# Kernel optimization log

Measured on AMD Instinct MI355X. Metric: run time of the kernel, lower is better.

The kernel has to match this reference:

```python
import math
import jax, jax.numpy as jnp
import numpy as np

D_MODEL = 1024
N_HEAD = 16
HEAD_DIM = D_MODEL // N_HEAD


def _alibi_slopes(n_heads: int) -> np.ndarray:
    def pow2_slopes(n):
        start = 2.0 ** (-(2.0 ** (-(math.log2(n) - 3))))
        return [start * (start ** i) for i in range(n)]
    if math.log2(n_heads).is_integer():
        slopes = pow2_slopes(n_heads)
    else:
        cp2 = 2 ** math.floor(math.log2(n_heads))
        slopes = pow2_slopes(cp2)
        slopes += pow2_slopes(2 * cp2)[0::2][: n_heads - cp2]
    return np.asarray(slopes, dtype=np.float32)


def setup_inputs() -> dict:
    key = jax.random.key(0)
    ks = jax.random.split(key, 12)
    B, N, D = 2, 2048, D_MODEL
    s = 1.0 / math.sqrt(D)
    inp = {
        "x_q": jax.random.normal(ks[0], (B, N, D), dtype=jnp.float32),
        "x_kv": jax.random.normal(ks[1], (B, N, D), dtype=jnp.float32),
        "attn_bias": jax.random.normal(ks[2], (N, N), dtype=jnp.float32) * 0.1,
        "Wq": jax.random.normal(ks[3], (D, D), dtype=jnp.float32) * s,
        "bq": jnp.zeros((D,), dtype=jnp.float32),
        "Wk": jax.random.normal(ks[4], (D, D), dtype=jnp.float32) * s,
        "bk": jnp.zeros((D,), dtype=jnp.float32),
        "Wv": jax.random.normal(ks[5], (D, D), dtype=jnp.float32) * s,
        "bv": jnp.zeros((D,), dtype=jnp.float32),
        "Wo": jax.random.normal(ks[6], (D, D), dtype=jnp.float32) * s,
        "bo": jnp.zeros((D,), dtype=jnp.float32),
        "is_self_attn": 1,
        "causal": 1,
    }
    return inp


def reference(x_q, x_kv, attn_bias, Wq, bq, Wk, bk, Wv, bv, Wo, bo, is_self_attn, causal):
    B, Nq, D = x_q.shape
    Nk = x_kv.shape[1]
    H, hd = N_HEAD, HEAD_DIM

    # torch Linear: y = x @ W.T + b
    q = (jnp.einsum("bqd,ed->bqe", x_q, Wq) + bq).reshape(B, Nq, H, hd)
    k = (jnp.einsum("bkd,ed->bke", x_kv, Wk) + bk).reshape(B, Nk, H, hd)
    v = (jnp.einsum("bkd,ed->bke", x_kv, Wv) + bv).reshape(B, Nk, H, hd)

    logits = jnp.einsum("bqhd,bkhd->bhqk", q, k) / math.sqrt(hd)  # [B,H,Nq,Nk]

    if is_self_attn and Nq == Nk:
        i = jnp.arange(Nq)[:, None]
        j = jnp.arange(Nk)[None, :]
        dist = jnp.maximum(j - i, 0).astype(jnp.float32)  # [Nq,Nk]
        slopes = jnp.asarray(_alibi_slopes(H))  # [H]
        logits = logits - slopes[None, :, None, None] * dist[None, None]

    if attn_bias is not None:
        logits = logits + attn_bias[None, None]

    if causal and is_self_attn and Nq == Nk:
        mask = jnp.triu(jnp.ones((Nq, Nk), dtype=bool), k=1)
        logits = jnp.where(mask[None, None], -jnp.inf, logits)

    attn = jax.nn.softmax(logits, axis=-1)
    out = jnp.einsum("bhqk,bkhd->bqhd", attn, v).reshape(B, Nq, D)
    return jnp.einsum("bqd,ed->bqe", out, Wo) + bo
```

## Files before the change

### kernel.cpp

```cpp
#include <hip/hip_runtime.h>
#include <hip/hip_bf16.h>

typedef __attribute__((ext_vector_type(8))) short short8;
typedef __attribute__((ext_vector_type(4))) float floatx4;

#define NSEQ   2048
#define DMODEL 1024
#define NHEAD  16
#define HDIM   64
#define BATCH  2
#define LOG2E 1.44269504088896340736f

#define XF4   1048576u
#define WF4   262144u

__device__ __forceinline__ void gload16(const void* g, void* l) {
    __builtin_amdgcn_global_load_lds(
        (const __attribute__((address_space(1))) void*)g,
        (__attribute__((address_space(3))) void*)l, 16, 0, 0);
}

#define BARRIER() asm volatile("s_barrier" ::: "memory")

__global__ __launch_bounds__(256)
void cvt_all(const float* __restrict__ xq, const float* __restrict__ xkv,
             const float* __restrict__ wq, const float* __restrict__ wk,
             const float* __restrict__ wv, const float* __restrict__ wo,
             __hip_bfloat16* __restrict__ dxq, __hip_bfloat16* __restrict__ dxkv,
             __hip_bfloat16* __restrict__ dwq, __hip_bfloat16* __restrict__ dwk,
             __hip_bfloat16* __restrict__ dwv, __hip_bfloat16* __restrict__ dwo)
{
    const unsigned total = 2*XF4 + 4*WF4;
    const unsigned stride = gridDim.x * blockDim.x;
    for (unsigned i = blockIdx.x*blockDim.x + threadIdx.x; i < total; i += stride) {
        const float4* src; __hip_bfloat16* dst; unsigned off;
        if (i < XF4)        { src = (const float4*)xq;  dst = dxq;  off = i; }
        else if (i < 2*XF4) { src = (const float4*)xkv; dst = dxkv; off = i - XF4; }
        else {
            unsigned j = i - 2*XF4; unsigned ws = j >> 18; off = j & (WF4 - 1);
            src = (const float4*)(ws==0 ? wq : ws==1 ? wk : ws==2 ? wv : wo);
            dst = (ws==0 ? dwq : ws==1 ? dwk : ws==2 ? dwv : dwo);
        }
        float4 v = src[off];
        __hip_bfloat16 h[4] = {__float2bfloat16(v.x), __float2bfloat16(v.y),
                               __float2bfloat16(v.z), __float2bfloat16(v.w)};
        *reinterpret_cast<uint2*>(dst + (size_t)off*4) = *reinterpret_cast<uint2*>(h);
    }
}

__global__ __launch_bounds__(256)
void cvt_bias(const float* __restrict__ src, __hip_bfloat16* __restrict__ dst)
{
    const unsigned total = (unsigned)(NSEQ*(size_t)NSEQ/4);
    const unsigned stride = gridDim.x * blockDim.x;
    for (unsigned i = blockIdx.x*blockDim.x + threadIdx.x; i < total; i += stride) {
        float4 v = ((const float4*)src)[i];
        __hip_bfloat16 h[4] = {__float2bfloat16(v.x), __float2bfloat16(v.y),
                               __float2bfloat16(v.z), __float2bfloat16(v.w)};
        *reinterpret_cast<uint2*>(dst + (size_t)i*4) = *reinterpret_cast<uint2*>(h);
    }
}

struct QkvArgs {
    const __hip_bfloat16* A[3];
    const __hip_bfloat16* W[3];
    const float*          bias[3];
    __hip_bfloat16*       out[3];
};

__global__ __launch_bounds__(256)
void qkv_gemm(QkvArgs args)
{
    __shared__ __hip_bfloat16 S[256][72];

    const int tid  = threadIdx.x;
    const int lane = tid & 63;
    const int wv   = tid >> 6;
    const int wm   = wv >> 1, wn = wv & 1;
    const int l15  = lane & 15, l4 = lane >> 4;
    const int m0   = blockIdx.x * 128;
    const int n0   = blockIdx.y * 128;
    const int z    = blockIdx.z;

    const __hip_bfloat16* __restrict__ A = args.A[z];
    const __hip_bfloat16* __restrict__ W = args.W[z];

    floatx4 acc[4][4] = {};

    for (int k0 = 0; k0 < DMODEL; k0 += 64) {
        #pragma unroll
        for (int it = 0; it < 4; ++it) {
            const int sI   = tid + 256 * it;
            const int row  = sI >> 2;
            const int colq = (sI & 3) * 16;
            const __hip_bfloat16* src = (it < 2)
                ? A + (size_t)(m0 + row) * DMODEL + k0 + colq
                : W + (size_t)(n0 + row - 128) * DMODEL + k0 + colq;
            const uint4* s4 = reinterpret_cast<const uint4*>(src);
            *reinterpret_cast<uint4*>(&S[row][colq])     = s4[0];
            *reinterpret_cast<uint4*>(&S[row][colq + 8]) = s4[1];
        }
        __syncthreads();

        #pragma unroll
        for (int kk = 0; kk < 64; kk += 32) {
            short8 af[4], bf[4];
            #pragma unroll
            for (int mi = 0; mi < 4; ++mi)
                af[mi] = *reinterpret_cast<const short8*>(&S[wm*64 + mi*16 + l15][kk + l4*8]);
            #pragma unroll
            for (int nj = 0; nj < 4; ++nj)
                bf[nj] = *reinterpret_cast<const short8*>(&S[128 + wn*64 + nj*16 + l15][kk + l4*8]);
            #pragma unroll
            for (int mi = 0; mi < 4; ++mi)
                #pragma unroll
                for (int nj = 0; nj < 4; ++nj)
                    acc[mi][nj] = __builtin_amdgcn_mfma_f32_16x16x32_bf16(
                        af[mi], bf[nj], acc[mi][nj], 0, 0, 0);
        }
        __syncthreads();
    }

    const float* bias = args.bias[z];
    __hip_bfloat16* C = args.out[z];
    const bool vt = (z == 2);
    #pragma unroll
    for (int mi = 0; mi < 4; ++mi) {
        const int mbase = m0 + wm*64 + mi*16 + l4*4;
        #pragma unroll
        for (int nj = 0; nj < 4; ++nj) {
            const int nn = n0 + wn*64 + nj*16 + l15;
            const float bb = bias[nn];
            const int h = nn >> 6, d = nn & (HDIM - 1);
            #pragma unroll
            for (int r = 0; r < 4; ++r) {
                const int m = mbase + r;
                const int b = m >> 11, n = m & (NSEQ - 1);
                const float val = acc[mi][nj][r] + bb;
                if (!vt)
                    C[((size_t)(b*NHEAD + h) * NSEQ + n) * HDIM + d] = __float2bfloat16(val);
                else
                    C[((size_t)(b*NHEAD + h) * HDIM + d) * NSEQ + n] = __float2bfloat16(val);
            }
        }
    }
}

__global__ __launch_bounds__(256)
void oproj_gemm(const __hip_bfloat16* __restrict__ A, const __hip_bfloat16* __restrict__ W,
                const float* __restrict__ bias, float* __restrict__ C)
{
    __shared__ __hip_bfloat16 S[192][72];

    const int tid  = threadIdx.x;
    const int lane = tid & 63;
    const int wv   = tid >> 6;
    const int l15  = lane & 15, l4 = lane >> 4;
    const int m0   = blockIdx.x * 64;
    const int n0   = blockIdx.y * 128;

    floatx4 acc[4][2] = {};

    for (int k0 = 0; k0 < DMODEL; k0 += 64) {
        #pragma unroll
        for (int it = 0; it < 3; ++it) {
            const int sI   = tid + 256 * it;
            const int row  = sI >> 2;
            const int colq = (sI & 3) * 16;
            const __hip_bfloat16* src = (it < 1)
                ? A + (size_t)(m0 + row) * DMODEL + k0 + colq
                : W + (size_t)(n0 + row - 64) * DMODEL + k0 + colq;
            const uint4* s4 = reinterpret_cast<const uint4*>(src);
            *reinterpret_cast<uint4*>(&S[row][colq])     = s4[0];
            *reinterpret_cast<uint4*>(&S[row][colq + 8]) = s4[1];
        }
        __syncthreads();

        #pragma unroll
        for (int kk = 0; kk < 64; kk += 32) {
            short8 af[4], bf[2];
            #pragma unroll
            for (int mi = 0; mi < 4; ++mi)
                af[mi] = *reinterpret_cast<const short8*>(&S[mi*16 + l15][kk + l4*8]);
            #pragma unroll
            for (int nj = 0; nj < 2; ++nj)
                bf[nj] = *reinterpret_cast<const short8*>(&S[64 + wv*32 + nj*16 + l15][kk + l4*8]);
            #pragma unroll
            for (int mi = 0; mi < 4; ++mi)
                #pragma unroll
                for (int nj = 0; nj < 2; ++nj)
                    acc[mi][nj] = __builtin_amdgcn_mfma_f32_16x16x32_bf16(
                        af[mi], bf[nj], acc[mi][nj], 0, 0, 0);
        }
        __syncthreads();
    }

    #pragma unroll
    for (int mi = 0; mi < 4; ++mi) {
        const int mbase = m0 + mi*16 + l4*4;
        #pragma unroll
        for (int nj = 0; nj < 2; ++nj) {
            const int nn = n0 + wv*32 + nj*16 + l15;
            const float bb = bias[nn];
            #pragma unroll
            for (int r = 0; r < 4; ++r)
                C[(size_t)(mbase + r) * DMODEL + nn] = acc[mi][nj][r] + bb;
        }
    }
}

__global__ __launch_bounds__(256)
void flash_attn(const __hip_bfloat16* __restrict__ Q,
                const __hip_bfloat16* __restrict__ K,
                const __hip_bfloat16* __restrict__ VT,
                const __hip_bfloat16* __restrict__ Bb,
                const int* __restrict__ selfp,
                const int* __restrict__ causalp,
                __hip_bfloat16* __restrict__ Oout)
{
    __shared__ __align__(16) char KB[2][8192];
    __shared__ __align__(16) char VB[2][8192];
    __shared__ __align__(16) char BBUF[2][8192];
    __shared__ __hip_bfloat16 pl[4][16][72];

    const int tid  = threadIdx.x;
    const int lane = tid & 63;
    const int wv   = tid >> 6;
    const int l15  = lane & 15, l4 = lane >> 4;

    const int g   = blockIdx.x;
    const int bh  = ((g >> 3) & 3) * 8 + (g & 7);
    const int m   = g >> 5;
    const int u   = m & 7, k2 = m >> 3;
    const int qb  = (k2==0) ? u : (k2==1) ? 31-u : (k2==2) ? 8+u : 23-u;
    const int h   = bh & (NHEAD - 1);
    const int b   = bh >> 4;

    const int selfF   = selfp[0];
    const int causalF = causalp[0];
    const bool cz      = (selfF != 0) && (causalF != 0);
    const bool alibiOn = (selfF != 0) && (causalF == 0);
    const float slopeL2 = exp2f(-(8.0f / NHEAD) * (float)(h + 1)) * LOG2E;

    const char* Kh = (const char*)(K  + (size_t)bh * NSEQ * HDIM);
    const char* Vh = (const char*)(VT + (size_t)bh * HDIM * NSEQ);
    const char* Bh = (const char*)(Bb + (size_t)qb * 64 * NSEQ);
    const __hip_bfloat16* Qh = Q + (size_t)bh * NSEQ * HDIM;

    const int q0 = qb*64 + wv*16;
    const short8 qf0 = *(const short8*)&Qh[(q0 + l15)*HDIM + l4*8];
    const short8 qf1 = *(const short8*)&Qh[(q0 + l15)*HDIM + 32 + l4*8];

    const int nt = cz ? (qb + 1) : (NSEQ/64);

    const int srow = lane >> 3;
    const int co   = (((lane & 7) ^ srow) << 4);

    auto stage = [&](int t, int bi) {
        const int j0 = t << 6;
        #pragma unroll
        for (int i2 = 0; i2 < 2; ++i2) {
            const int rl = wv*16 + i2*8 + srow;
            const int db = (wv*16 + i2*8) * 128;
            gload16(Kh + (size_t)(j0 + rl)*128 + co,          &KB[bi][db]);
            gload16(Vh + (size_t)rl*4096 + (size_t)j0*2 + co, &VB[bi][db]);
            gload16(Bh + (size_t)rl*4096 + (size_t)j0*2 + co, &BBUF[bi][db]);
        }
    };

    floatx4 o[4] = {};
    float lr[4] = {0.f, 0.f, 0.f, 0.f};

    stage(0, 0);
    int cur = 0;
    for (int t = 0; t < nt; ++t) {
        if (t + 1 < nt) {
            stage(t + 1, cur ^ 1);
            asm volatile("s_waitcnt vmcnt(6)" ::: "memory");
        } else {
            asm volatile("s_waitcnt vmcnt(0)" ::: "memory");
        }
        BARRIER();

        const char* kb = KB[cur];
        const char* vb = VB[cur];
        const char* bb = BBUF[cur];

        floatx4 s4[4];
        #pragma unroll
        for (int tt = 0; tt < 4; ++tt) {
            const int row = tt*16 + l15;
            const int sw  = (row & 7) << 4;
            const short8 kf0 = *(const short8*)(kb + ((row*128 + l4*16)      ^ sw));
            const short8 kf1 = *(const short8*)(kb + ((row*128 + 64 + l4*16) ^ sw));
            floatx4 z = {};
            z      = __builtin_amdgcn_mfma_f32_16x16x32_bf16(qf0, kf0, z, 0, 0, 0);
            s4[tt] = __builtin_amdgcn_mfma_f32_16x16x32_bf16(qf1, kf1, z, 0, 0, 0);
        }

        const bool domask = cz && (t == nt - 1);
        #pragma unroll
        for (int tt = 0; tt < 4; ++tt) {
            #pragma unroll
            for (int r = 0; r < 4; ++r) {
                const int qloc = wv*16 + l4*4 + r;
                const int jloc = tt*16 + l15;
                const int bbyte = (qloc*128 + jloc*2) ^ ((qloc & 7) << 4);
                const unsigned short ub = *(const unsigned short*)(bb + bbyte);
                union { unsigned int i; float f; } cvu; cvu.i = ((unsigned)ub) << 16;
                float v2 = fmaf(s4[tt][r], 0.125f * LOG2E, cvu.f * LOG2E);
                if (alibiOn) {
                    const int dd = (t*64 + jloc) - (qb*64 + qloc);
                    if (dd > 0) v2 = fmaf((float)dd, -slopeL2, v2);
                }
                float e = __builtin_amdgcn_exp2f(v2);
                if (domask && jloc > qloc) e = 0.0f;
                lr[r] += e;
                pl[wv][l4*4 + r][tt*16 + l15] = __float2bfloat16(e);
            }
        }

        const short8 pf0 = *(const short8*)&pl[wv][l15][l4*8];
        const short8 pf1 = *(const short8*)&pl[wv][l15][32 + l4*8];

        #pragma unroll
        for (int dt = 0; dt < 4; ++dt) {
            const int row = dt*16 + l15;
            const int sw  = (row & 7) << 4;
            const short8 vf0 = *(const short8*)(vb + ((row*128 + l4*16)      ^ sw));
            const short8 vf1 = *(const short8*)(vb + ((row*128 + 64 + l4*16) ^ sw));
            o[dt] = __builtin_amdgcn_mfma_f32_16x16x32_bf16(pf0, vf0, o[dt], 0, 0, 0);
            o[dt] = __builtin_amdgcn_mfma_f32_16x16x32_bf16(pf1, vf1, o[dt], 0, 0, 0);
        }

        BARRIER();
        cur ^= 1;
    }

    #pragma unroll
    for (int msk = 1; msk < 16; msk <<= 1)
        #pragma unroll
        for (int r = 0; r < 4; ++r)
            lr[r] += __shfl_xor(lr[r], msk);

    #pragma unroll
    for (int r = 0; r < 4; ++r) {
        const float inv = 1.0f / lr[r];
        const int n = qb*64 + wv*16 + l4*4 + r;
        #pragma unroll
        for (int dt = 0; dt < 4; ++dt)
            Oout[((size_t)(b*NSEQ + n)) * DMODEL + h*HDIM + dt*16 + l15] =
                __float2bfloat16(o[dt][r] * inv);
    }
}

extern "C" void kernel_launch(void* const* d_in, const int* in_sizes, int n_in,
                              void* d_out, int out_size, void* d_ws, size_t ws_size,
                              hipStream_t stream)
{
    (void)in_sizes; (void)n_in; (void)out_size; (void)ws_size;
    const float* x_q  = (const float*)d_in[0];
    const float* x_kv = (const float*)d_in[1];
    const float* ab   = (const float*)d_in[2];
    const float* Wq   = (const float*)d_in[3];
    const float* bq   = (const float*)d_in[4];
    const float* Wk   = (const float*)d_in[5];
    const float* bk   = (const float*)d_in[6];
    const float* Wv   = (const float*)d_in[7];
    const float* bv   = (const float*)d_in[8];
    const float* Wo   = (const float*)d_in[9];
    const float* bo   = (const float*)d_in[10];
    const int* selfp   = (const int*)d_in[11];
    const int* causalp = (const int*)d_in[12];

    const size_t XB = (size_t)BATCH * NSEQ * DMODEL * sizeof(__hip_bfloat16);
    const size_t WB = (size_t)DMODEL * DMODEL * sizeof(__hip_bfloat16);
    char* ws = (char*)d_ws;
    __hip_bfloat16* xq_b  = (__hip_bfloat16*)(ws);
    __hip_bfloat16* AO    = (__hip_bfloat16*)(ws);
    __hip_bfloat16* xkv_b = (__hip_bfloat16*)(ws + XB);
    __hip_bfloat16* ab_b  = (__hip_bfloat16*)(ws + XB);
    __hip_bfloat16* Wq_b  = (__hip_bfloat16*)(ws + 2*XB);
    __hip_bfloat16* Wk_b  = (__hip_bfloat16*)(ws + 2*XB + WB);
    __hip_bfloat16* Wv_b  = (__hip_bfloat16*)(ws + 2*XB + 2*WB);
    __hip_bfloat16* Wo_b  = (__hip_bfloat16*)(ws + 2*XB + 3*WB);
    __hip_bfloat16* Qb    = (__hip_bfloat16*)(ws + 2*XB + 4*WB);
    __hip_bfloat16* Kb    = (__hip_bfloat16*)(ws + 2*XB + 4*WB + XB);
    __hip_bfloat16* VTb   = (__hip_bfloat16*)(ws + 2*XB + 4*WB + 2*XB);

    cvt_all<<<dim3(2048), dim3(256), 0, stream>>>(
        x_q, x_kv, Wq, Wk, Wv, Wo, xq_b, xkv_b, Wq_b, Wk_b, Wv_b, Wo_b);

    QkvArgs qa;
    qa.A[0] = xq_b;  qa.A[1] = xkv_b; qa.A[2] = xkv_b;
    qa.W[0] = Wq_b;  qa.W[1] = Wk_b;  qa.W[2] = Wv_b;
    qa.bias[0] = bq; qa.bias[1] = bk; qa.bias[2] = bv;
    qa.out[0] = Qb;  qa.out[1] = Kb;  qa.out[2] = VTb;
    qkv_gemm<<<dim3(32, 8, 3), dim3(256), 0, stream>>>(qa);

    cvt_bias<<<dim3(1024), dim3(256), 0, stream>>>(ab, ab_b);

    flash_attn<<<dim3(1024), dim3(256), 0, stream>>>(
        Qb, Kb, VTb, ab_b, selfp, causalp, AO);

    oproj_gemm<<<dim3(64, 8), dim3(256), 0, stream>>>(AO, Wo_b, bo, (float*)d_out);
}
```

Before: 154.3 us.

## Pair causal query blocks per workgroup for balanced attention work

```diff
diff --git a/kernel.cpp b/kernel.cpp
--- a/kernel.cpp
+++ b/kernel.cpp
@@ -55,8 +55,8 @@
     const unsigned stride = gridDim.x * blockDim.x;
     for (unsigned i = blockIdx.x*blockDim.x + threadIdx.x; i < total; i += stride) {
         float4 v = ((const float4*)src)[i];
-        __hip_bfloat16 h[4] = {__float2bfloat16(v.x), __float2bfloat16(v.y),
-                               __float2bfloat16(v.z), __float2bfloat16(v.w)};
+        __hip_bfloat16 h[4] = {__float2bfloat16(v.x * LOG2E), __float2bfloat16(v.y * LOG2E),
+                               __float2bfloat16(v.z * LOG2E), __float2bfloat16(v.w * LOG2E)};
         *reinterpret_cast<uint2*>(dst + (size_t)i*4) = *reinterpret_cast<uint2*>(h);
     }
 }
@@ -229,10 +229,9 @@
     const int l15  = lane & 15, l4 = lane >> 4;
 
     const int g   = blockIdx.x;
-    const int bh  = ((g >> 3) & 3) * 8 + (g & 7);
-    const int m   = g >> 5;
-    const int u   = m & 7, k2 = m >> 3;
-    const int qb  = (k2==0) ? u : (k2==1) ? 31-u : (k2==2) ? 8+u : 23-u;
+    const int bh  = g & 31;
+    const int u   = g >> 5;
+    const int qA  = u, qB = 31 - u;
     const int h   = bh & (NHEAD - 1);
     const int b   = bh >> 4;
 
@@ -244,20 +243,25 @@
 
     const char* Kh = (const char*)(K  + (size_t)bh * NSEQ * HDIM);
     const char* Vh = (const char*)(VT + (size_t)bh * HDIM * NSEQ);
-    const char* Bh = (const char*)(Bb + (size_t)qb * 64 * NSEQ);
     const __hip_bfloat16* Qh = Q + (size_t)bh * NSEQ * HDIM;
 
-    const int q0 = qb*64 + wv*16;
-    const short8 qf0 = *(const short8*)&Qh[(q0 + l15)*HDIM + l4*8];
-    const short8 qf1 = *(const short8*)&Qh[(q0 + l15)*HDIM + 32 + l4*8];
-
-    const int nt = cz ? (qb + 1) : (NSEQ/64);
+    const int nA = cz ? (qA + 1) : (NSEQ/64);
+    const int NT = cz ? 33 : (NSEQ/32);
+
+    const int qa0 = qA*64 + wv*16, qb0 = qB*64 + wv*16;
+    const short8 qfA0 = *(const short8*)&Qh[(qa0 + l15)*HDIM + l4*8];
+    const short8 qfA1 = *(const short8*)&Qh[(qa0 + l15)*HDIM + 32 + l4*8];
+    const short8 qfB0 = *(const short8*)&Qh[(qb0 + l15)*HDIM + l4*8];
+    const short8 qfB1 = *(const short8*)&Qh[(qb0 + l15)*HDIM + 32 + l4*8];
 
     const int srow = lane >> 3;
     const int co   = (((lane & 7) ^ srow) << 4);
 
-    auto stage = [&](int t, int bi) {
-        const int j0 = t << 6;
+    auto stage = [&](int it, int bi) {
+        int qq, jt;
+        if (it < nA) { qq = qA; jt = it; } else { qq = qB; jt = it - nA; }
+        const int j0 = jt << 6;
+        const char* Bh = (const char*)Bb + (size_t)qq * 64 * (NSEQ*2);
         #pragma unroll
         for (int i2 = 0; i2 < 2; ++i2) {
             const int rl = wv*16 + i2*8 + srow;
@@ -270,12 +274,14 @@
 
     floatx4 o[4] = {};
     float lr[4] = {0.f, 0.f, 0.f, 0.f};
+    short8 qf0 = qfA0, qf1 = qfA1;
+    int qbc = qA;
 
     stage(0, 0);
     int cur = 0;
-    for (int t = 0; t < nt; ++t) {
-        if (t + 1 < nt) {
-            stage(t + 1, cur ^ 1);
+    for (int it = 0; it < NT; ++it) {
+        if (it + 1 < NT) {
+            stage(it + 1, cur ^ 1);
             asm volatile("s_waitcnt vmcnt(6)" ::: "memory");
         } else {
             asm volatile("s_waitcnt vmcnt(0)" ::: "memory");
@@ -285,8 +291,10 @@
         const char* kb = KB[cur];
         const char* vb = VB[cur];
         const char* bb = BBUF[cur];
+        const int jt = (it < nA) ? it : it - nA;
 
         floatx4 s4[4];
+        __builtin_amdgcn_s_setprio(1);
         #pragma unroll
         for (int tt = 0; tt < 4; ++tt) {
             const int row = tt*16 + l15;
@@ -297,8 +305,9 @@
             z      = __builtin_amdgcn_mfma_f32_16x16x32_bf16(qf0, kf0, z, 0, 0, 0);
             s4[tt] = __builtin_amdgcn_mfma_f32_16x16x32_bf16(qf1, kf1, z, 0, 0, 0);
         }
-
-        const bool domask = cz && (t == nt - 1);
+        __builtin_amdgcn_s_setprio(0);
+
+        const bool domask = cz && (it == nA - 1 || it == NT - 1);
         #pragma unroll
         for (int tt = 0; tt < 4; ++tt) {
             #pragma unroll
@@ -308,9 +317,9 @@
                 const int bbyte = (qloc*128 + jloc*2) ^ ((qloc & 7) << 4);
                 const unsigned short ub = *(const unsigned short*)(bb + bbyte);
                 union { unsigned int i; float f; } cvu; cvu.i = ((unsigned)ub) << 16;
-                float v2 = fmaf(s4[tt][r], 0.125f * LOG2E, cvu.f * LOG2E);
+                float v2 = fmaf(s4[tt][r], 0.125f * LOG2E, cvu.f);
                 if (alibiOn) {
-                    const int dd = (t*64 + jloc) - (qb*64 + qloc);
+                    const int dd = (jt*64 + jloc) - (qbc*64 + qloc);
                     if (dd > 0) v2 = fmaf((float)dd, -slopeL2, v2);
                 }
                 float e = __builtin_amdgcn_exp2f(v2);
@@ -323,6 +332,7 @@
         const short8 pf0 = *(const short8*)&pl[wv][l15][l4*8];
         const short8 pf1 = *(const short8*)&pl[wv][l15][32 + l4*8];
 
+        __builtin_amdgcn_s_setprio(1);
         #pragma unroll
         for (int dt = 0; dt < 4; ++dt) {
             const int row = dt*16 + l15;
@@ -332,25 +342,34 @@
             o[dt] = __builtin_amdgcn_mfma_f32_16x16x32_bf16(pf0, vf0, o[dt], 0, 0, 0);
             o[dt] = __builtin_amdgcn_mfma_f32_16x16x32_bf16(pf1, vf1, o[dt], 0, 0, 0);
         }
+        __builtin_amdgcn_s_setprio(0);
 
         BARRIER();
         cur ^= 1;
-    }
-
-    #pragma unroll
-    for (int msk = 1; msk < 16; msk <<= 1)
-        #pragma unroll
-        for (int r = 0; r < 4; ++r)
-            lr[r] += __shfl_xor(lr[r], msk);
-
-    #pragma unroll
-    for (int r = 0; r < 4; ++r) {
-        const float inv = 1.0f / lr[r];
-        const int n = qb*64 + wv*16 + l4*4 + r;
-        #pragma unroll
-        for (int dt = 0; dt < 4; ++dt)
-            Oout[((size_t)(b*NSEQ + n)) * DMODEL + h*HDIM + dt*16 + l15] =
-                __float2bfloat16(o[dt][r] * inv);
+
+        if (it == nA - 1 || it == NT - 1) {
+            #pragma unroll
+            for (int msk = 1; msk < 16; msk <<= 1)
+                #pragma unroll
+                for (int r = 0; r < 4; ++r)
+                    lr[r] += __shfl_xor(lr[r], msk);
+            #pragma unroll
+            for (int r = 0; r < 4; ++r) {
+                const float inv = 1.0f / lr[r];
+                const int n = qbc*64 + wv*16 + l4*4 + r;
+                #pragma unroll
+                for (int dt = 0; dt < 4; ++dt)
+                    Oout[((size_t)(b*NSEQ + n)) * DMODEL + h*HDIM + dt*16 + l15] =
+                        __float2bfloat16(o[dt][r] * inv);
+            }
+            if (it == nA - 1) {
+                #pragma unroll
+                for (int dt = 0; dt < 4; ++dt) o[dt] = floatx4{0.f, 0.f, 0.f, 0.f};
+                #pragma unroll
+                for (int r = 0; r < 4; ++r) lr[r] = 0.f;
+                qf0 = qfB0; qf1 = qfB1; qbc = qB;
+            }
+        }
     }
 }
 
@@ -400,7 +419,7 @@
 
     cvt_bias<<<dim3(1024), dim3(256), 0, stream>>>(ab, ab_b);
 
-    flash_attn<<<dim3(1024), dim3(256), 0, stream>>>(
+    flash_attn<<<dim3(512), dim3(256), 0, stream>>>(
         Qb, Kb, VTb, ab_b, selfp, causalp, AO);
 
     oproj_gemm<<<dim3(64, 8), dim3(256), 0, stream>>>(AO, Wo_b, bo, (float*)d_out);
```

Result: faster. 145.3 us (-5.8%).
